# Kernel optimization log

Measured on AMD Instinct MI355X. Metric: run time of the kernel, lower is better.

Reference implementation:

```python
import jax, jax.numpy as jnp
import numpy as np

EPS = 1e-05


def setup_inputs() -> dict:
    key = jax.random.key(0)
    ks = jax.random.split(key, 4)
    B, N, D, H, E = 16, 8192, 128, 64, 64
    x = jax.random.normal(ks[0], (B, N, D), dtype=jnp.float32)
    ln_w = jnp.ones((D,), jnp.float32)
    ln_b = jnp.zeros((D,), jnp.float32)
    Wl = jax.random.normal(ks[1], (D, H), dtype=jnp.float32) / np.sqrt(D)
    bl = jnp.zeros((H,), jnp.float32)
    Wr = jax.random.normal(ks[2], (D, H), dtype=jnp.float32) / np.sqrt(D)
    br = jnp.zeros((H,), jnp.float32)
    Wo = jax.random.normal(ks[3], (H, E), dtype=jnp.float32) / np.sqrt(H)
    bo = jnp.zeros((E,), jnp.float32)
    return {"x": x, "ln_w": ln_w, "ln_b": ln_b, "Wl": Wl, "bl": bl,
            "Wr": Wr, "br": br, "Wo": Wo, "bo": bo}


def _layernorm(x, w, b):
    mu = jnp.mean(x, axis=-1, keepdims=True)
    var = jnp.mean(jnp.square(x - mu), axis=-1, keepdims=True)
    return (x - mu) * jax.lax.rsqrt(var + EPS) * w + b


def reference(x, ln_w, ln_b, Wl, bl, Wr, br, Wo, bo):
    # x: [B, N, D]
    xn = _layernorm(x, ln_w, ln_b)
    left = xn @ Wl + bl    # [B, N, H]
    right = xn @ Wr + br   # [B, N, H]
    # Original: einsum('b i d, b j d -> b i j d').mean(dim=1).
    # Identical math without the O(N^2) tensor: mean over i factors out of
    # the product since left[b,i,d]*right[b,j,d] is separable in i.
    outer = left.mean(axis=1)[:, None, :] * right  # [B, N, H]
    return outer @ Wo + bo  # [B, N, E]
```

## Files before the change

kernel.cpp:

```cpp
#include <hip/hip_runtime.h>
#include <math.h>

#define B_  16
#define N_  8192
#define D_  128
#define H_  64
#define E_  64
#define EPSLN 1e-5f

typedef __attribute__((ext_vector_type(8))) short short8;
typedef __attribute__((ext_vector_type(4))) short short4v;
typedef __attribute__((ext_vector_type(4))) float f32x4;

#define WSB_PART 0
#define WSB_MT   1048576
#define WSB_T    1310720
#define WSB_C    1314816
#define WSB_MURS 1318912

static __device__ __forceinline__ unsigned short f2bf(float f) {
    union { float f; unsigned u; } c; c.f = f;
    unsigned u = c.u;
    return (unsigned short)((u + 0x7FFFu + ((u >> 16) & 1u)) >> 16);
}

__global__ __launch_bounds__(256) void k_stats(const float* __restrict__ x,
                                               float* __restrict__ partial,
                                               float2* __restrict__ murs) {
    __shared__ float xs[64 * 132];
    __shared__ float mul[64], rsl[64], red[128];
    int b = blockIdx.y, t = threadIdx.x;
    int rowbase = blockIdx.x * 64;
    size_t gbase = (size_t)(b * N_ + rowbase) * 32;

    const float4* x4 = (const float4*)x;
#pragma unroll
    for (int k = 0; k < 8; ++k) {
        int idx = t + 256 * k;
        int row = idx >> 5, c4 = idx & 31;
        *(float4*)&xs[row * 132 + c4 * 4] = x4[gbase + idx];
    }
    __syncthreads();

    {
        int r = t >> 2, q = t & 3;
        float s = 0.f, s2 = 0.f;
#pragma unroll
        for (int i = 0; i < 8; ++i) {
            float4 v = *(const float4*)&xs[r * 132 + q * 32 + i * 4];
            s  += (v.x + v.y) + (v.z + v.w);
            s2 += (v.x * v.x + v.y * v.y) + (v.z * v.z + v.w * v.w);
        }
        s  += __shfl_xor(s, 1, 64);  s  += __shfl_xor(s, 2, 64);
        s2 += __shfl_xor(s2, 1, 64); s2 += __shfl_xor(s2, 2, 64);
        if (q == 0) {
            float mu  = s * (1.f / D_);
            float var = s2 * (1.f / D_) - mu * mu;
            mul[r] = mu;
            rsl[r] = rsqrtf(var + EPSLN);
        }
    }
    __syncthreads();

    if (t < 64) {
        float2 mr; mr.x = mul[t]; mr.y = rsl[t];
        murs[(size_t)b * N_ + rowbase + t] = mr;
    }

    int c = t & 127, hh = t >> 7;
    float acc = 0.f;
#pragma unroll 8
    for (int i = 0; i < 32; ++i) {
        int r = hh * 32 + i;
        acc += rsl[r] * (xs[r * 132 + c] - mul[r]);
    }
    if (hh == 1) red[c] = acc;
    __syncthreads();
    if (hh == 0)
        partial[((size_t)b * 128 + blockIdx.x) * D_ + c] = acc + red[c];
}

__global__ __launch_bounds__(256) void k_combine(const float* __restrict__ partial,
                                                 const float* __restrict__ ln_w,
                                                 const float* __restrict__ ln_b,
                                                 const float* __restrict__ Wl,
                                                 const float* __restrict__ bl,
                                                 const float* __restrict__ Wr,
                                                 const float* __restrict__ br,
                                                 const float* __restrict__ Wo,
                                                 const float* __restrict__ bo,
                                                 unsigned short* __restrict__ Mt,
                                                 float* __restrict__ Tg,
                                                 float* __restrict__ Cg) {
    int b = blockIdx.y, dblk = blockIdx.x, t = threadIdx.x;
    __shared__ float cm[D_], ml[H_], uu[H_], qq[H_];
    __shared__ float P[H_ * E_];
    __shared__ float red2[256];

    {
        int d = t & 127, hhf = t >> 7;
        float sacc = 0.f;
        for (int j = hhf * 64; j < hhf * 64 + 64; ++j)
            sacc += partial[((size_t)b * 128 + j) * D_ + d];
        red2[t] = sacc;
    }
    __syncthreads();
    if (t < D_) cm[t] = ln_w[t] * (red2[t] + red2[t + 128]) * (1.f / N_) + ln_b[t];
    __syncthreads();

    if (t < H_) {
        float a = bl[t], u = 0.f, q = 0.f;
        for (int d = 0; d < D_; ++d) {
            float wr = Wr[d * H_ + t];
            a += cm[d] * Wl[d * H_ + t];
            u += ln_w[d] * wr;
            q += ln_b[d] * wr;
        }
        ml[t] = a; uu[t] = u; qq[t] = q + br[t];
    }
    __syncthreads();

#pragma unroll
    for (int k = 0; k < 16; ++k) {
        int idx = t + 256 * k;
        P[idx] = ml[idx >> 6] * Wo[idx];
    }
    __syncthreads();

    int d  = dblk * 32 + (t >> 3);
    int eo = (t & 7) * 8;
    float a0 = 0, a1 = 0, a2 = 0, a3 = 0, a4 = 0, a5 = 0, a6 = 0, a7 = 0;
    for (int h = 0; h < H_; ++h) {
        float wr = Wr[d * H_ + h];
        const float4* p4 = (const float4*)&P[h * E_ + eo];
        float4 pa = p4[0], pb = p4[1];
        a0 += wr * pa.x; a1 += wr * pa.y; a2 += wr * pa.z; a3 += wr * pa.w;
        a4 += wr * pb.x; a5 += wr * pb.y; a6 += wr * pb.z; a7 += wr * pb.w;
    }
    float wd = ln_w[d];
    size_t mb = (size_t)b * E_ * D_;
    Mt[mb + (size_t)(eo + 0) * D_ + d] = f2bf(wd * a0);
    Mt[mb + (size_t)(eo + 1) * D_ + d] = f2bf(wd * a1);
    Mt[mb + (size_t)(eo + 2) * D_ + d] = f2bf(wd * a2);
    Mt[mb + (size_t)(eo + 3) * D_ + d] = f2bf(wd * a3);
    Mt[mb + (size_t)(eo + 4) * D_ + d] = f2bf(wd * a4);
    Mt[mb + (size_t)(eo + 5) * D_ + d] = f2bf(wd * a5);
    Mt[mb + (size_t)(eo + 6) * D_ + d] = f2bf(wd * a6);
    Mt[mb + (size_t)(eo + 7) * D_ + d] = f2bf(wd * a7);

    if (dblk == 0 && t < E_) {
        float T = 0.f, C = bo[t];
        for (int h = 0; h < H_; ++h) {
            float p = P[h * E_ + t];
            T += uu[h] * p;
            C += qq[h] * p;
        }
        Tg[b * E_ + t] = T;
        Cg[b * E_ + t] = C;
    }
}

__global__ __launch_bounds__(256, 2) void k_gemm3(const float* __restrict__ x,
                                                  const float2* __restrict__ murs,
                                                  const unsigned short* __restrict__ Mt,
                                                  const float* __restrict__ Tg,
                                                  const float* __restrict__ Cg,
                                                  float* __restrict__ out) {
    __shared__ short xs[256 * 128];
    __shared__ float muL[256], rsL[256], Tl[E_], Cl[E_];

    int b = blockIdx.y, bx = blockIdx.x, t = threadIdx.x;
    int rowbase = bx * 256;

    if (t < E_) { Tl[t] = Tg[b * E_ + t]; Cl[t] = Cg[b * E_ + t]; }
    {
        float2 mr = murs[(size_t)b * N_ + rowbase + t];
        muL[t] = mr.x; rsL[t] = mr.y;
    }

    const float4* x4 = (const float4*)x;
    size_t gbase = (size_t)(b * N_ + rowbase) * 32;

    for (int kk = 0; kk < 4; ++kk) {
#pragma unroll
        for (int k = 0; k < 8; ++k) {
            int idx = t + 256 * (kk * 8 + k);
            int row = idx >> 5, c4 = idx & 31;
            float4 v = x4[gbase + idx];
            short4v sv;
            sv[0] = (short)f2bf(v.x); sv[1] = (short)f2bf(v.y);
            sv[2] = (short)f2bf(v.z); sv[3] = (short)f2bf(v.w);
            int g2 = c4 >> 1, half = c4 & 1;
            *(short4v*)&xs[row * 128 + ((g2 ^ (row & 15)) << 3) + (half << 2)] = sv;
        }
    }
    __syncthreads();

    int wv = t >> 6, lane = t & 63;
    int m16 = lane & 15, quad = lane >> 4;

    f32x4 acc[4][4];
#pragma unroll
    for (int i = 0; i < 4; ++i)
#pragma unroll
        for (int j = 0; j < 4; ++j) acc[i][j] = (f32x4){0.f, 0.f, 0.f, 0.f};

    const unsigned short* Mb = Mt + (size_t)b * E_ * D_;

#pragma unroll
    for (int kc = 0; kc < 4; ++kc) {
        short8 af[4], bf[4];
#pragma unroll
        for (int mt = 0; mt < 4; ++mt) {
            int row = wv * 64 + mt * 16 + m16;
            int g = kc * 4 + quad;
            af[mt] = *(const short8*)&xs[row * 128 + ((g ^ m16) * 8)];
        }
#pragma unroll
        for (int nt = 0; nt < 4; ++nt) {
            bf[nt] = *(const short8*)(Mb + (size_t)(nt * 16 + m16) * D_ + kc * 32 + quad * 8);
        }
#pragma unroll
        for (int mt = 0; mt < 4; ++mt)
#pragma unroll
            for (int nt = 0; nt < 4; ++nt)
                acc[mt][nt] = __builtin_amdgcn_mfma_f32_16x16x32_bf16(
                    af[mt], bf[nt], acc[mt][nt], 0, 0, 0);
    }

    size_t outbase = (size_t)(b * N_ + rowbase) * E_;
#pragma unroll
    for (int mt = 0; mt < 4; ++mt) {
        int rb = wv * 64 + mt * 16 + quad * 4;
        float mu0 = muL[rb + 0], rs0 = rsL[rb + 0];
        float mu1 = muL[rb + 1], rs1 = rsL[rb + 1];
        float mu2 = muL[rb + 2], rs2 = rsL[rb + 2];
        float mu3 = muL[rb + 3], rs3 = rsL[rb + 3];
#pragma unroll
        for (int nt = 0; nt < 4; ++nt) {
            int col = nt * 16 + m16;
            float Tc = Tl[col], Cc = Cl[col];
            float* o = out + outbase + (size_t)rb * E_ + col;
            o[0 * E_] = rs0 * (acc[mt][nt][0] - mu0 * Tc) + Cc;
            o[1 * E_] = rs1 * (acc[mt][nt][1] - mu1 * Tc) + Cc;
            o[2 * E_] = rs2 * (acc[mt][nt][2] - mu2 * Tc) + Cc;
            o[3 * E_] = rs3 * (acc[mt][nt][3] - mu3 * Tc) + Cc;
        }
    }
}

extern "C" void kernel_launch(void* const* d_in, const int* in_sizes, int n_in,
                              void* d_out, int out_size, void* d_ws, size_t ws_size,
                              hipStream_t stream) {
    const float* x    = (const float*)d_in[0];
    const float* ln_w = (const float*)d_in[1];
    const float* ln_b = (const float*)d_in[2];
    const float* Wl   = (const float*)d_in[3];
    const float* bl   = (const float*)d_in[4];
    const float* Wr   = (const float*)d_in[5];
    const float* br   = (const float*)d_in[6];
    const float* Wo   = (const float*)d_in[7];
    const float* bo   = (const float*)d_in[8];
    float* out = (float*)d_out;
    char* ws   = (char*)d_ws;

    float*          partial = (float*)(ws + WSB_PART);
    unsigned short* Mt      = (unsigned short*)(ws + WSB_MT);
    float*          Tg      = (float*)(ws + WSB_T);
    float*          Cg      = (float*)(ws + WSB_C);
    float2*         murs    = (float2*)(ws + WSB_MURS);

    k_stats<<<dim3(128, 16), dim3(256), 0, stream>>>(x, partial, murs);

    k_combine<<<dim3(4, 16), dim3(256), 0, stream>>>(partial, ln_w, ln_b, Wl, bl,
                                                     Wr, br, Wo, bo, Mt, Tg, Cg);

    k_gemm3<<<dim3(32, 16), dim3(256), 0, stream>>>(x, murs, Mt, Tg, Cg, out);
}
```

Measured before the change: 153.1 us.

## Fuse combine into stats via last-block atomic counter; widen GEMM blocks to 512 threads

The combine kernel is merged into the stats kernel. Each block bumps a per-batch atomic counter, and the last block to finish for a batch does the reduction and builds the bf16 Mt, T and C data, looping over all four d-blocks itself. The aim is to remove one kernel launch and its dependency gap. The cost is that the combine work for each batch now runs in a single block, and a memset is needed to clear the counters. Separately, the GEMM kernel moves to 512 threads with 8 waves of 32 rows each, to hide load latency better.

```diff
diff --git a/kernel.cpp b/kernel.cpp
--- a/kernel.cpp
+++ b/kernel.cpp
@@ -17,6 +17,7 @@
 #define WSB_T    1310720
 #define WSB_C    1314816
 #define WSB_MURS 1318912
+#define WSB_CNT  2367488
 
 static __device__ __forceinline__ unsigned short f2bf(float f) {
     union { float f; unsigned u; } c; c.f = f;
@@ -24,11 +25,24 @@
     return (unsigned short)((u + 0x7FFFu + ((u >> 16) & 1u)) >> 16);
 }
 
-__global__ __launch_bounds__(256) void k_stats(const float* __restrict__ x,
-                                               float* __restrict__ partial,
-                                               float2* __restrict__ murs) {
-    __shared__ float xs[64 * 132];
-    __shared__ float mul[64], rsl[64], red[128];
+__global__ __launch_bounds__(256, 4) void k_stats(
+    const float* __restrict__ x,
+    const float* __restrict__ ln_w, const float* __restrict__ ln_b,
+    const float* __restrict__ Wl,   const float* __restrict__ bl,
+    const float* __restrict__ Wr,   const float* __restrict__ br,
+    const float* __restrict__ Wo,   const float* __restrict__ bo,
+    float* __restrict__ partial, float2* __restrict__ murs,
+    unsigned* __restrict__ cnt,
+    unsigned short* __restrict__ Mt,
+    float* __restrict__ Tg, float* __restrict__ Cg)
+{
+    __shared__ float smem[64 * 132 + 64 + 64 + 128];
+    __shared__ int   isLast;
+    float* xs  = smem;
+    float* mul = smem + 8448;
+    float* rsl = smem + 8512;
+    float* red = smem + 8576;
+
     int b = blockIdx.y, t = threadIdx.x;
     int rowbase = blockIdx.x * 64;
     size_t gbase = (size_t)(b * N_ + rowbase) * 32;
@@ -67,35 +81,34 @@
         murs[(size_t)b * N_ + rowbase + t] = mr;
     }
 
-    int c = t & 127, hh = t >> 7;
-    float acc = 0.f;
+    {
+        int c = t & 127, hh = t >> 7;
+        float acc = 0.f;
 #pragma unroll 8
-    for (int i = 0; i < 32; ++i) {
-        int r = hh * 32 + i;
-        acc += rsl[r] * (xs[r * 132 + c] - mul[r]);
-    }
-    if (hh == 1) red[c] = acc;
-    __syncthreads();
-    if (hh == 0)
-        partial[((size_t)b * 128 + blockIdx.x) * D_ + c] = acc + red[c];
-}
-
-__global__ __launch_bounds__(256) void k_combine(const float* __restrict__ partial,
-                                                 const float* __restrict__ ln_w,
-                                                 const float* __restrict__ ln_b,
-                                                 const float* __restrict__ Wl,
-                                                 const float* __restrict__ bl,
-                                                 const float* __restrict__ Wr,
-                                                 const float* __restrict__ br,
-                                                 const float* __restrict__ Wo,
-                                                 const float* __restrict__ bo,
-                                                 unsigned short* __restrict__ Mt,
-                                                 float* __restrict__ Tg,
-                                                 float* __restrict__ Cg) {
-    int b = blockIdx.y, dblk = blockIdx.x, t = threadIdx.x;
-    __shared__ float cm[D_], ml[H_], uu[H_], qq[H_];
-    __shared__ float P[H_ * E_];
-    __shared__ float red2[256];
+        for (int i = 0; i < 32; ++i) {
+            int r = hh * 32 + i;
+            acc += rsl[r] * (xs[r * 132 + c] - mul[r]);
+        }
+        if (hh == 1) red[c] = acc;
+        __syncthreads();
+        if (hh == 0)
+            partial[((size_t)b * 128 + blockIdx.x) * D_ + c] = acc + red[c];
+    }
+
+    __threadfence();
+    __syncthreads();
+    if (t == 0) isLast = (atomicAdd(&cnt[b], 1u) == 127u);
+    __syncthreads();
+    if (!isLast) return;
+    __threadfence();
+    __syncthreads();
+
+    float* P    = smem;
+    float* cm   = smem + 4096;
+    float* ml   = smem + 4224;
+    float* uu   = smem + 4288;
+    float* qq   = smem + 4352;
+    float* red2 = smem + 4416;
 
     {
         int d = t & 127, hhf = t >> 7;
@@ -127,28 +140,30 @@
     }
     __syncthreads();
 
-    int d  = dblk * 32 + (t >> 3);
-    int eo = (t & 7) * 8;
-    float a0 = 0, a1 = 0, a2 = 0, a3 = 0, a4 = 0, a5 = 0, a6 = 0, a7 = 0;
-    for (int h = 0; h < H_; ++h) {
-        float wr = Wr[d * H_ + h];
-        const float4* p4 = (const float4*)&P[h * E_ + eo];
-        float4 pa = p4[0], pb = p4[1];
-        a0 += wr * pa.x; a1 += wr * pa.y; a2 += wr * pa.z; a3 += wr * pa.w;
-        a4 += wr * pb.x; a5 += wr * pb.y; a6 += wr * pb.z; a7 += wr * pb.w;
-    }
-    float wd = ln_w[d];
-    size_t mb = (size_t)b * E_ * D_;
-    Mt[mb + (size_t)(eo + 0) * D_ + d] = f2bf(wd * a0);
-    Mt[mb + (size_t)(eo + 1) * D_ + d] = f2bf(wd * a1);
-    Mt[mb + (size_t)(eo + 2) * D_ + d] = f2bf(wd * a2);
-    Mt[mb + (size_t)(eo + 3) * D_ + d] = f2bf(wd * a3);
-    Mt[mb + (size_t)(eo + 4) * D_ + d] = f2bf(wd * a4);
-    Mt[mb + (size_t)(eo + 5) * D_ + d] = f2bf(wd * a5);
-    Mt[mb + (size_t)(eo + 6) * D_ + d] = f2bf(wd * a6);
-    Mt[mb + (size_t)(eo + 7) * D_ + d] = f2bf(wd * a7);
-
-    if (dblk == 0 && t < E_) {
+    for (int dblk = 0; dblk < 4; ++dblk) {
+        int d  = dblk * 32 + (t >> 3);
+        int eo = (t & 7) * 8;
+        float a0 = 0, a1 = 0, a2 = 0, a3 = 0, a4 = 0, a5 = 0, a6 = 0, a7 = 0;
+        for (int h = 0; h < H_; ++h) {
+            float wr = Wr[d * H_ + h];
+            const float4* p4 = (const float4*)&P[h * E_ + eo];
+            float4 pa = p4[0], pb = p4[1];
+            a0 += wr * pa.x; a1 += wr * pa.y; a2 += wr * pa.z; a3 += wr * pa.w;
+            a4 += wr * pb.x; a5 += wr * pb.y; a6 += wr * pb.z; a7 += wr * pb.w;
+        }
+        float wd = ln_w[d];
+        size_t mb = (size_t)b * E_ * D_;
+        Mt[mb + (size_t)(eo + 0) * D_ + d] = f2bf(wd * a0);
+        Mt[mb + (size_t)(eo + 1) * D_ + d] = f2bf(wd * a1);
+        Mt[mb + (size_t)(eo + 2) * D_ + d] = f2bf(wd * a2);
+        Mt[mb + (size_t)(eo + 3) * D_ + d] = f2bf(wd * a3);
+        Mt[mb + (size_t)(eo + 4) * D_ + d] = f2bf(wd * a4);
+        Mt[mb + (size_t)(eo + 5) * D_ + d] = f2bf(wd * a5);
+        Mt[mb + (size_t)(eo + 6) * D_ + d] = f2bf(wd * a6);
+        Mt[mb + (size_t)(eo + 7) * D_ + d] = f2bf(wd * a7);
+    }
+
+    if (t < E_) {
         float T = 0.f, C = bo[t];
         for (int h = 0; h < H_; ++h) {
             float p = P[h * E_ + t];
@@ -160,7 +175,7 @@
     }
 }
 
-__global__ __launch_bounds__(256, 2) void k_gemm3(const float* __restrict__ x,
+__global__ __launch_bounds__(512, 4) void k_gemm4(const float* __restrict__ x,
                                                   const float2* __restrict__ murs,
                                                   const unsigned short* __restrict__ Mt,
                                                   const float* __restrict__ Tg,
@@ -173,7 +188,7 @@
     int rowbase = bx * 256;
 
     if (t < E_) { Tl[t] = Tg[b * E_ + t]; Cl[t] = Cg[b * E_ + t]; }
-    {
+    if (t < 256) {
         float2 mr = murs[(size_t)b * N_ + rowbase + t];
         muL[t] = mr.x; rsL[t] = mr.y;
     }
@@ -181,27 +196,25 @@
     const float4* x4 = (const float4*)x;
     size_t gbase = (size_t)(b * N_ + rowbase) * 32;
 
-    for (int kk = 0; kk < 4; ++kk) {
-#pragma unroll
-        for (int k = 0; k < 8; ++k) {
-            int idx = t + 256 * (kk * 8 + k);
-            int row = idx >> 5, c4 = idx & 31;
-            float4 v = x4[gbase + idx];
-            short4v sv;
-            sv[0] = (short)f2bf(v.x); sv[1] = (short)f2bf(v.y);
-            sv[2] = (short)f2bf(v.z); sv[3] = (short)f2bf(v.w);
-            int g2 = c4 >> 1, half = c4 & 1;
-            *(short4v*)&xs[row * 128 + ((g2 ^ (row & 15)) << 3) + (half << 2)] = sv;
-        }
+#pragma unroll
+    for (int k = 0; k < 16; ++k) {
+        int idx = t + 512 * k;
+        int row = idx >> 5, c4 = idx & 31;
+        float4 v = x4[gbase + idx];
+        short4v sv;
+        sv[0] = (short)f2bf(v.x); sv[1] = (short)f2bf(v.y);
+        sv[2] = (short)f2bf(v.z); sv[3] = (short)f2bf(v.w);
+        int g2 = c4 >> 1, half = c4 & 1;
+        *(short4v*)&xs[row * 128 + ((g2 ^ (row & 15)) << 3) + (half << 2)] = sv;
     }
     __syncthreads();
 
     int wv = t >> 6, lane = t & 63;
     int m16 = lane & 15, quad = lane >> 4;
 
-    f32x4 acc[4][4];
-#pragma unroll
-    for (int i = 0; i < 4; ++i)
+    f32x4 acc[2][4];
+#pragma unroll
+    for (int i = 0; i < 2; ++i)
 #pragma unroll
         for (int j = 0; j < 4; ++j) acc[i][j] = (f32x4){0.f, 0.f, 0.f, 0.f};
 
@@ -209,10 +222,10 @@
 
 #pragma unroll
     for (int kc = 0; kc < 4; ++kc) {
-        short8 af[4], bf[4];
-#pragma unroll
-        for (int mt = 0; mt < 4; ++mt) {
-            int row = wv * 64 + mt * 16 + m16;
+        short8 af[2], bf[4];
+#pragma unroll
+        for (int mt = 0; mt < 2; ++mt) {
+            int row = wv * 32 + mt * 16 + m16;
             int g = kc * 4 + quad;
             af[mt] = *(const short8*)&xs[row * 128 + ((g ^ m16) * 8)];
         }
@@ -221,7 +234,7 @@
             bf[nt] = *(const short8*)(Mb + (size_t)(nt * 16 + m16) * D_ + kc * 32 + quad * 8);
         }
 #pragma unroll
-        for (int mt = 0; mt < 4; ++mt)
+        for (int mt = 0; mt < 2; ++mt)
 #pragma unroll
             for (int nt = 0; nt < 4; ++nt)
                 acc[mt][nt] = __builtin_amdgcn_mfma_f32_16x16x32_bf16(
@@ -230,8 +243,8 @@
 
     size_t outbase = (size_t)(b * N_ + rowbase) * E_;
 #pragma unroll
-    for (int mt = 0; mt < 4; ++mt) {
-        int rb = wv * 64 + mt * 16 + quad * 4;
+    for (int mt = 0; mt < 2; ++mt) {
+        int rb = wv * 32 + mt * 16 + quad * 4;
         float mu0 = muL[rb + 0], rs0 = rsL[rb + 0];
         float mu1 = muL[rb + 1], rs1 = rsL[rb + 1];
         float mu2 = muL[rb + 2], rs2 = rsL[rb + 2];
@@ -269,11 +282,13 @@
     float*          Tg      = (float*)(ws + WSB_T);
     float*          Cg      = (float*)(ws + WSB_C);
     float2*         murs    = (float2*)(ws + WSB_MURS);
-
-    k_stats<<<dim3(128, 16), dim3(256), 0, stream>>>(x, partial, murs);
-
-    k_combine<<<dim3(4, 16), dim3(256), 0, stream>>>(partial, ln_w, ln_b, Wl, bl,
-                                                     Wr, br, Wo, bo, Mt, Tg, Cg);
-
-    k_gemm3<<<dim3(32, 16), dim3(256), 0, stream>>>(x, murs, Mt, Tg, Cg, out);
-}
+    unsigned*       cnt     = (unsigned*)(ws + WSB_CNT);
+
+    hipMemsetAsync(cnt, 0, B_ * sizeof(unsigned), stream);
+
+    k_stats<<<dim3(128, 16), dim3(256), 0, stream>>>(
+        x, ln_w, ln_b, Wl, bl, Wr, br, Wo, bo,
+        partial, murs, cnt, Mt, Tg, Cg);
+
+    k_gemm4<<<dim3(32, 16), dim3(512), 0, stream>>>(x, murs, Mt, Tg, Cg, out);
+}
```

Measured after the change: 355.7 us. +132.3%, slower.
